# Performance work log

Measured on AMD Instinct MI355X. Metric: run time of the kernel, lower is better.

The kernel has to match this reference:

```python
import jax, jax.numpy as jnp
import numpy as np

CC = 0.25  # commitment cost
K1 = 4096
K2 = 4096
D1 = 64
D2 = 64

def conv1d(x, w, b, stride=1, pad=0):
    # x: [N,C,T], w: [O,I,K] (torch layout)
    y = jax.lax.conv_general_dilated(x, w, (stride,), [(pad, pad)],
                                     dimension_numbers=('NCH', 'OIH', 'NCH'))
    return y + b[None, :, None]

def convT1d(x, w, b, stride=2, pad=1):
    # torch ConvTranspose1d weight layout: [Cin, Cout, K]
    k = w.shape[-1]
    w2 = jnp.flip(w, -1).transpose(1, 0, 2)  # -> [Cout, Cin, K]
    y = jax.lax.conv_general_dilated(x, w2, (1,), [(k - 1 - pad, k - 1 - pad)],
                                     lhs_dilation=(stride,),
                                     dimension_numbers=('NCH', 'OIH', 'NCH'))
    return y + b[None, :, None]

def resblocks(x, w1, b1, w2, b2):
    # w1: [n, C, C, 3], w2: [n, C, C, 1]; n is small & fixed (2)
    for i in range(w1.shape[0]):
        h = conv1d(jax.nn.relu(x), w1[i], b1[i], 1, 1)
        h = conv1d(jax.nn.relu(h), w2[i], b2[i], 1, 0)
        x = x + h
    return x

def quantize(x, embed):
    # x: [B,D,T]; embed: [K,D]
    b, d, t = x.shape
    xf = x.transpose(0, 2, 1).reshape(-1, d)               # [N,D]
    dist = (xf * xf).sum(1, keepdims=True) - 2.0 * (xf @ embed.T) + (embed * embed).sum(1)
    idx = jnp.argmin(dist, axis=1)                          # [N]
    q = embed[idx]                                          # gather == onehot @ embed
    commit = CC * jnp.mean((jax.lax.stop_gradient(q) - xf) ** 2)
    q = xf + jax.lax.stop_gradient(q - xf)                  # straight-through
    q = q.reshape(b, t, d).transpose(0, 2, 1)
    K = embed.shape[0]
    avg = jnp.zeros(K, xf.dtype).at[idx].add(1.0) / xf.shape[0]
    perp = jnp.exp(-jnp.sum(avg * jnp.log(avg + 1e-10)))
    usage = jnp.sum(avg * jnp.log(avg * K + 1e-10))
    return q, commit, perp, usage

def setup_inputs() -> dict:
    key = jax.random.key(0)
    ks = iter(jax.random.split(key, 64))
    def p(*shape):
        return jax.random.normal(next(ks), shape, jnp.float32) * 0.05
    inp = {}
    inp['x'] = jax.random.normal(next(ks), (16, 1, 8192), jnp.float32)
    c1, c2, c3 = 128, 256, 384
    # Encoder
    inp['e_c1_w'] = p(c1, 1, 7);   inp['e_c1_b'] = p(c1)
    inp['e_r1_w1'] = p(2, c1, c1, 3); inp['e_r1_b1'] = p(2, c1)
    inp['e_r1_w2'] = p(2, c1, c1, 1); inp['e_r1_b2'] = p(2, c1)
    inp['e_c2_w'] = p(c2, c1, 5);  inp['e_c2_b'] = p(c2)
    inp['e_r2_w1'] = p(2, c2, c2, 3); inp['e_r2_b1'] = p(2, c2)
    inp['e_r2_w2'] = p(2, c2, c2, 1); inp['e_r2_b2'] = p(2, c2)
    inp['e_c3_w'] = p(c3, c2, 3);  inp['e_c3_b'] = p(c3)
    inp['e_r3_w1'] = p(2, c3, c3, 3); inp['e_r3_b1'] = p(2, c3)
    inp['e_r3_w2'] = p(2, c3, c3, 1); inp['e_r3_b2'] = p(2, c3)
    inp['e_pr_w'] = p(128, c3, 1); inp['e_pr_b'] = p(128)
    # Codebooks (torch.randn init)
    inp['emb1'] = jax.random.normal(next(ks), (K1, D1), jnp.float32)
    inp['emb2'] = jax.random.normal(next(ks), (K2, D2), jnp.float32)
    # Decoder
    inp['d_pr_w'] = p(c3, 128, 1); inp['d_pr_b'] = p(c3)
    inp['d_r1_w1'] = p(2, c3, c3, 3); inp['d_r1_b1'] = p(2, c3)
    inp['d_r1_w2'] = p(2, c3, c3, 1); inp['d_r1_b2'] = p(2, c3)
    inp['d_u1_w'] = p(c3, c2, 4);  inp['d_u1_b'] = p(c2)  # ConvTranspose: [Cin,Cout,K]
    inp['d_r2_w1'] = p(2, c2, c2, 3); inp['d_r2_b1'] = p(2, c2)
    inp['d_r2_w2'] = p(2, c2, c2, 1); inp['d_r2_b2'] = p(2, c2)
    inp['d_u2_w'] = p(c2, c1, 4);  inp['d_u2_b'] = p(c1)
    inp['d_r3_w1'] = p(2, c1, c1, 3); inp['d_r3_b1'] = p(2, c1)
    inp['d_r3_w2'] = p(2, c1, c1, 1); inp['d_r3_b2'] = p(2, c1)
    inp['d_u3_w'] = p(c1, c1, 4);  inp['d_u3_b'] = p(c1)
    inp['d_out_w'] = p(1, c1, 7);  inp['d_out_b'] = p(1)
    return inp

def reference(x, e_c1_w, e_c1_b, e_r1_w1, e_r1_b1, e_r1_w2, e_r1_b2,
              e_c2_w, e_c2_b, e_r2_w1, e_r2_b1, e_r2_w2, e_r2_b2,
              e_c3_w, e_c3_b, e_r3_w1, e_r3_b1, e_r3_w2, e_r3_b2,
              e_pr_w, e_pr_b, emb1, emb2,
              d_pr_w, d_pr_b, d_r1_w1, d_r1_b1, d_r1_w2, d_r1_b2,
              d_u1_w, d_u1_b, d_r2_w1, d_r2_b1, d_r2_w2, d_r2_b2,
              d_u2_w, d_u2_b, d_r3_w1, d_r3_b1, d_r3_w2, d_r3_b2,
              d_u3_w, d_u3_b, d_out_w, d_out_b):
    # Encoder
    z = conv1d(x, e_c1_w, e_c1_b, stride=2, pad=3)
    z = resblocks(z, e_r1_w1, e_r1_b1, e_r1_w2, e_r1_b2)
    z = conv1d(z, e_c2_w, e_c2_b, stride=2, pad=2)
    z = resblocks(z, e_r2_w1, e_r2_b1, e_r2_w2, e_r2_b2)
    z = conv1d(z, e_c3_w, e_c3_b, stride=2, pad=1)
    z = resblocks(z, e_r3_w1, e_r3_b1, e_r3_w2, e_r3_b2)
    z = conv1d(z, e_pr_w, e_pr_b)
    # Product VQ
    q1, c1l, p1, u1 = quantize(z[:, :D1], emb1)
    q2, c2l, p2, u2 = quantize(z[:, D1:], emb2)
    q = jnp.concatenate([q1, q2], axis=1)
    # Decoder
    h = conv1d(q, d_pr_w, d_pr_b)
    h = resblocks(h, d_r1_w1, d_r1_b1, d_r1_w2, d_r1_b2)
    h = convT1d(h, d_u1_w, d_u1_b)
    h = resblocks(h, d_r2_w1, d_r2_b1, d_r2_w2, d_r2_b2)
    h = convT1d(h, d_u2_w, d_u2_b)
    h = resblocks(h, d_r3_w1, d_r3_b1, d_r3_w2, d_r3_b2)
    h = convT1d(h, d_u3_w, d_u3_b)
    x_hat = conv1d(h, d_out_w, d_out_b, stride=1, pad=3)
    return (x_hat, c1l + c2l, u1 + u2, p1, p2)
```

## Files before the change

### kernel.cpp

```cpp
#include <hip/hip_runtime.h>
#include <math.h>

#define TPB 256
typedef __bf16 bf16x8 __attribute__((ext_vector_type(8)));
typedef float f32x4 __attribute__((ext_vector_type(4)));

static __device__ __forceinline__ float bf2f(unsigned short h) {
    union { unsigned int u; float f; } x; x.u = ((unsigned int)h) << 16; return x.f;
}
static __device__ __forceinline__ unsigned short f2bf(float f) {
    union { float f; unsigned int u; } x; x.f = f;
    unsigned int r = x.u + 0x7FFFu + ((x.u >> 16) & 1u);
    return (unsigned short)(r >> 16);
}
static __device__ __forceinline__ unsigned int relu_pk(unsigned int v) {
    unsigned int hi = (v & 0x80000000u) ? 0u : (v & 0xFFFF0000u);
    unsigned int lo = (v & 0x8000u) ? 0u : (v & 0xFFFFu);
    return hi | lo;
}
static __device__ __forceinline__ f32x4 MFMA(bf16x8 a, bf16x8 b, f32x4 c) {
    return __builtin_amdgcn_mfma_f32_16x16x32_bf16(a, b, c, 0, 0, 0);
}

template<int K, bool RELU>
__global__ __launch_bounds__(TPB) void conv1d_k(
    const float* __restrict__ x, const float* __restrict__ w,
    const float* __restrict__ bias, const float* __restrict__ res,
    float* __restrict__ y,
    int N, int Ci, int T, int Co, int To, int stride, int pad)
{
    int id = blockIdx.x * TPB + threadIdx.x;
    int total = N * Co * To;
    if (id >= total) return;
    int to = id % To;
    int co = (id / To) % Co;
    int n  = id / (To * Co);
    const float* xn = x + (size_t)n * Ci * T;
    const float* wc = w + (size_t)co * Ci * K;
    float acc = bias[co];
    int h0 = to * stride - pad;
    for (int ci = 0; ci < Ci; ++ci) {
        const float* xc = xn + (size_t)ci * T;
        const float* wk = wc + (size_t)ci * K;
        #pragma unroll
        for (int k = 0; k < K; ++k) {
            int pos = h0 + k;
            if (pos >= 0 && pos < T) {
                float v = xc[pos];
                if (RELU) v = fmaxf(v, 0.0f);
                acc = fmaf(v, wk[k], acc);
            }
        }
    }
    if (res) acc += res[id];
    y[id] = acc;
}

template<int K, int S, bool RELU, bool RES>
__global__ __launch_bounds__(TPB) void conv_tile_k(
    const float* __restrict__ x, const float* __restrict__ w,
    const float* __restrict__ bias, const float* __restrict__ res,
    float* __restrict__ y, int Ci, int Ti, int Co, int To)
{
    constexpr int CC    = 16;
    constexpr int TNEED = 127 * S + K;
    constexpr int RS    = ((TNEED + 3) & ~3) + 4;
    constexpr int NXV   = 7 * S + K;
    constexpr int NV4   = (NXV + 3) / 4;
    constexpr int WROW  = 68;
    __shared__ float xs[CC][RS];
    __shared__ float ws[CC * K * WROW];

    const int tid   = threadIdx.x;
    const int co_g  = tid & 15;
    const int t_g   = tid >> 4;
    const int tg8S  = t_g * 8 * S;
    const int co_g4 = co_g * 4;
    const int n     = blockIdx.z;
    const int co0   = blockIdx.y * 64;
    const int tb    = blockIdx.x * 128;
    const int t0in  = tb * S - K / 2;

    float4 b4 = *(const float4*)&bias[co0 + co_g4];
    float bi[4] = {b4.x, b4.y, b4.z, b4.w};
    float acc[4][8];
    #pragma unroll
    for (int i = 0; i < 4; ++i)
        #pragma unroll
        for (int j = 0; j < 8; ++j) acc[i][j] = bi[i];

    const int nchunk = Ci / CC;
    for (int ch = 0; ch < nchunk; ++ch) {
        const int ci0 = ch * CC;
        __syncthreads();
        for (int lin = tid; lin < CC * TNEED; lin += TPB) {
            int r = lin / TNEED, off = lin - r * TNEED;
            int t = t0in + off;
            float v = 0.f;
            if (t >= 0 && t < Ti) {
                v = x[((size_t)(n * Ci + ci0 + r)) * Ti + t];
                if (RELU) v = fmaxf(v, 0.f);
            }
            xs[r][off] = v;
        }
        for (int lin = tid; lin < 64 * CC * K; lin += TPB) {
            int co_l = lin / (CC * K), rem = lin - co_l * (CC * K);
            ws[rem * WROW + co_l] =
                w[(size_t)(co0 + co_l) * Ci * K + (size_t)ci0 * K + rem];
        }
        __syncthreads();
        for (int r = 0; r < CC; ++r) {
            float xv[NV4 * 4];
            #pragma unroll
            for (int q = 0; q < NV4; ++q)
                *(float4*)&xv[q * 4] = *(const float4*)&xs[r][tg8S + q * 4];
            #pragma unroll
            for (int k = 0; k < K; ++k) {
                float4 wv = *(const float4*)&ws[(r * K + k) * WROW + co_g4];
                float wa[4] = {wv.x, wv.y, wv.z, wv.w};
                #pragma unroll
                for (int i = 0; i < 4; ++i)
                    #pragma unroll
                    for (int j = 0; j < 8; ++j)
                        acc[i][j] = fmaf(wa[i], xv[j * S + k], acc[i][j]);
            }
        }
    }
    #pragma unroll
    for (int i = 0; i < 4; ++i) {
        size_t yb = ((size_t)(n * Co + co0 + co_g4 + i)) * To + tb + t_g * 8;
        float4 lo = make_float4(acc[i][0], acc[i][1], acc[i][2], acc[i][3]);
        float4 hi = make_float4(acc[i][4], acc[i][5], acc[i][6], acc[i][7]);
        if (RES) {
            float4 r0 = *(const float4*)&res[yb];
            float4 r1 = *(const float4*)&res[yb + 4];
            lo.x += r0.x; lo.y += r0.y; lo.z += r0.z; lo.w += r0.w;
            hi.x += r1.x; hi.y += r1.y; hi.z += r1.z; hi.w += r1.w;
        }
        *(float4*)&y[yb]     = lo;
        *(float4*)&y[yb + 4] = hi;
    }
}

template<int K, int TOFF, bool RELU, bool RES, int OSTR, int OOFF>
__global__ __launch_bounds__(TPB) void gconv_k(
    const unsigned short* __restrict__ x, const unsigned short* __restrict__ wp,
    const float* __restrict__ bias, const unsigned short* __restrict__ res,
    unsigned short* __restrict__ y, int Ci, int Tin, int Co, int Tout)
{
    constexpr int XR = 64 + K - 1;
    __shared__ unsigned short x_lds[XR * 40];
    __shared__ unsigned short w_lds[K * 64 * 40];
    const int tid = threadIdx.x;
    const int n = blockIdx.z, co0 = blockIdx.y * 64, P = blockIdx.x * 64;
    const int wid = tid >> 6, l = tid & 63;
    const int wm = wid >> 1, wn = wid & 1;
    const int lr = l & 15, kg = l >> 4;
    f32x4 acc[2][2] = {{{0.f,0.f,0.f,0.f},{0.f,0.f,0.f,0.f}},
                       {{0.f,0.f,0.f,0.f},{0.f,0.f,0.f,0.f}}};
    const int nch = Ci >> 5;
    for (int cc = 0; cc < nch; ++cc) {
        __syncthreads();
        for (int i = tid; i < XR * 4; i += TPB) {
            int r = i >> 2, c4 = i & 3;
            int gr = P + TOFF + r;
            uint4 v = make_uint4(0u, 0u, 0u, 0u);
            if (gr >= 0 && gr < Tin)
                v = *(const uint4*)(x + ((size_t)(n * Tin + gr) * Ci + cc * 32 + c4 * 8));
            if (RELU) { v.x = relu_pk(v.x); v.y = relu_pk(v.y);
                        v.z = relu_pk(v.z); v.w = relu_pk(v.w); }
            *(uint4*)&x_lds[r * 40 + c4 * 8] = v;
        }
        for (int i = tid; i < K * 64 * 4; i += TPB) {
            int r2 = i >> 2, c4 = i & 3;
            *(uint4*)&w_lds[r2 * 40 + c4 * 8] =
                *(const uint4*)(wp + ((size_t)((r2 >> 6) * Co + co0 + (r2 & 63)) * Ci
                                      + cc * 32 + c4 * 8));
        }
        __syncthreads();
        #pragma unroll
        for (int kk = 0; kk < K; ++kk) {
            bf16x8 av0 = *(const bf16x8*)&x_lds[(wm * 32 +      lr + kk) * 40 + kg * 8];
            bf16x8 av1 = *(const bf16x8*)&x_lds[(wm * 32 + 16 + lr + kk) * 40 + kg * 8];
            bf16x8 bv0 = *(const bf16x8*)&w_lds[(kk * 64 + wn * 32 +      lr) * 40 + kg * 8];
            bf16x8 bv1 = *(const bf16x8*)&w_lds[(kk * 64 + wn * 32 + 16 + lr) * 40 + kg * 8];
            acc[0][0] = MFMA(av0, bv0, acc[0][0]);
            acc[0][1] = MFMA(av0, bv1, acc[0][1]);
            acc[1][0] = MFMA(av1, bv0, acc[1][0]);
            acc[1][1] = MFMA(av1, bv1, acc[1][1]);
        }
    }
    float bb[2] = { bias[co0 + wn * 32 + lr], bias[co0 + wn * 32 + 16 + lr] };
    #pragma unroll
    for (int mf = 0; mf < 2; ++mf)
        #pragma unroll
        for (int nf = 0; nf < 2; ++nf) {
            int co = co0 + wn * 32 + nf * 16 + lr;
            #pragma unroll
            for (int r = 0; r < 4; ++r) {
                int m = wm * 32 + mf * 16 + kg * 4 + r;
                int orow = (P + m) * OSTR + OOFF;
                float v = acc[mf][nf][r] + bb[nf];
                size_t oidx = ((size_t)n * Tout + orow) * Co + co;
                if (RES) v += bf2f(res[oidx]);
                y[oidx] = f2bf(v);
            }
        }
}

__global__ __launch_bounds__(TPB) void gconvt_k(
    const unsigned short* __restrict__ x, const unsigned short* __restrict__ wpe,
    const unsigned short* __restrict__ wpo, const float* __restrict__ bias,
    unsigned short* __restrict__ y, int Ci, int Tin, int Co)
{
    __shared__ unsigned short x_lds[66 * 40];
    __shared__ unsigned short we_lds[2 * 64 * 40];
    __shared__ unsigned short wo_lds[2 * 64 * 40];
    const int tid = threadIdx.x;
    const int n = blockIdx.z, co0 = blockIdx.y * 64, P = blockIdx.x * 64;
    const int wid = tid >> 6, l = tid & 63;
    const int wm = wid >> 1, wn = wid & 1;
    const int lr = l & 15, kg = l >> 4;
    f32x4 accE[2][2] = {{{0.f,0.f,0.f,0.f},{0.f,0.f,0.f,0.f}},
                        {{0.f,0.f,0.f,0.f},{0.f,0.f,0.f,0.f}}};
    f32x4 accO[2][2] = {{{0.f,0.f,0.f,0.f},{0.f,0.f,0.f,0.f}},
                        {{0.f,0.f,0.f,0.f},{0.f,0.f,0.f,0.f}}};
    const int nch = Ci >> 5;
    for (int cc = 0; cc < nch; ++cc) {
        __syncthreads();
        for (int i = tid; i < 66 * 4; i += TPB) {
            int r = i >> 2, c4 = i & 3;
            int gr = P - 1 + r;
            uint4 v = make_uint4(0u, 0u, 0u, 0u);
            if (gr >= 0 && gr < Tin)
                v = *(const uint4*)(x + ((size_t)(n * Tin + gr) * Ci + cc * 32 + c4 * 8));
            *(uint4*)&x_lds[r * 40 + c4 * 8] = v;
        }
        for (int i = tid; i < 2 * 64 * 4; i += TPB) {
            int r2 = i >> 2, c4 = i & 3;
            size_t off = (size_t)((r2 >> 6) * Co + co0 + (r2 & 63)) * Ci + cc * 32 + c4 * 8;
            *(uint4*)&we_lds[r2 * 40 + c4 * 8] = *(const uint4*)(wpe + off);
            *(uint4*)&wo_lds[r2 * 40 + c4 * 8] = *(const uint4*)(wpo + off);
        }
        __syncthreads();
        #pragma unroll
        for (int kk = 0; kk < 2; ++kk) {
            bf16x8 aE0 = *(const bf16x8*)&x_lds[(wm * 32 +      lr + kk) * 40 + kg * 8];
            bf16x8 aE1 = *(const bf16x8*)&x_lds[(wm * 32 + 16 + lr + kk) * 40 + kg * 8];
            bf16x8 bE0 = *(const bf16x8*)&we_lds[(kk * 64 + wn * 32 +      lr) * 40 + kg * 8];
            bf16x8 bE1 = *(const bf16x8*)&we_lds[(kk * 64 + wn * 32 + 16 + lr) * 40 + kg * 8];
            accE[0][0] = MFMA(aE0, bE0, accE[0][0]);
            accE[0][1] = MFMA(aE0, bE1, accE[0][1]);
            accE[1][0] = MFMA(aE1, bE0, accE[1][0]);
            accE[1][1] = MFMA(aE1, bE1, accE[1][1]);
            bf16x8 aO0 = *(const bf16x8*)&x_lds[(wm * 32 +      lr + kk + 1) * 40 + kg * 8];
            bf16x8 aO1 = *(const bf16x8*)&x_lds[(wm * 32 + 16 + lr + kk + 1) * 40 + kg * 8];
            bf16x8 bO0 = *(const bf16x8*)&wo_lds[(kk * 64 + wn * 32 +      lr) * 40 + kg * 8];
            bf16x8 bO1 = *(const bf16x8*)&wo_lds[(kk * 64 + wn * 32 + 16 + lr) * 40 + kg * 8];
            accO[0][0] = MFMA(aO0, bO0, accO[0][0]);
            accO[0][1] = MFMA(aO0, bO1, accO[0][1]);
            accO[1][0] = MFMA(aO1, bO0, accO[1][0]);
            accO[1][1] = MFMA(aO1, bO1, accO[1][1]);
        }
    }
    float bb[2] = { bias[co0 + wn * 32 + lr], bias[co0 + wn * 32 + 16 + lr] };
    #pragma unroll
    for (int mf = 0; mf < 2; ++mf)
        #pragma unroll
        for (int nf = 0; nf < 2; ++nf) {
            int co = co0 + wn * 32 + nf * 16 + lr;
            #pragma unroll
            for (int r = 0; r < 4; ++r) {
                int m = wm * 32 + mf * 16 + kg * 4 + r;
                size_t oe = ((size_t)n * (2 * Tin) + (size_t)(P + m) * 2) * Co + co;
                y[oe]      = f2bf(accE[mf][nf][r] + bb[nf]);
                y[oe + Co] = f2bf(accO[mf][nf][r] + bb[nf]);
            }
        }
}

__global__ __launch_bounds__(TPB) void prep_conv_k(
    const float* __restrict__ w, unsigned short* __restrict__ out, int Co, int Ci, int K)
{
    int id = blockIdx.x * TPB + threadIdx.x;
    if (id >= K * Co * Ci) return;
    int ci = id % Ci, co = (id / Ci) % Co, k = id / (Ci * Co);
    out[id] = f2bf(w[((size_t)co * Ci + ci) * K + k]);
}
__global__ __launch_bounds__(TPB) void prep_convt_k(
    const float* __restrict__ w, unsigned short* __restrict__ oute,
    unsigned short* __restrict__ outo, int Co, int Ci)
{
    int id = blockIdx.x * TPB + threadIdx.x;
    if (id >= 2 * Co * Ci) return;
    int ci = id % Ci, co = (id / Ci) % Co, kp = id / (Ci * Co);
    const float* src = w + ((size_t)ci * Co + co) * 4;
    oute[id] = f2bf(src[3 - 2 * kp]);
    outo[id] = f2bf(src[2 - 2 * kp]);
}

__global__ __launch_bounds__(TPB) void dout_cl_k(
    const unsigned short* __restrict__ x, const float* __restrict__ w,
    const float* __restrict__ b, float* __restrict__ y)
{
    __shared__ unsigned short xs[262 * 40];
    const int tid = threadIdx.x;
    const int tb = blockIdx.x * 256;
    const int n = blockIdx.y;
    float acc = b[0];
    for (int cc = 0; cc < 4; ++cc) {
        __syncthreads();
        for (int i = tid; i < 262 * 4; i += TPB) {
            int r = i >> 2, c4 = i & 3;
            int gr = tb - 3 + r;
            uint4 v = make_uint4(0u, 0u, 0u, 0u);
            if (gr >= 0 && gr < 8192)
                v = *(const uint4*)(x + ((size_t)(n * 8192 + gr) * 128 + cc * 32 + c4 * 8));
            *(uint4*)&xs[r * 40 + c4 * 8] = v;
        }
        __syncthreads();
        #pragma unroll
        for (int k = 0; k < 7; ++k) {
            const unsigned short* row = &xs[(tid + k) * 40];
            #pragma unroll
            for (int e = 0; e < 32; ++e)
                acc = fmaf(bf2f(row[e]), w[(cc * 32 + e) * 7 + k], acc);
        }
    }
    y[(size_t)n * 8192 + tb + tid] = acc;
}

#define NVEC 16384
#define KC   4096
#define DD   64
#define NCH  16

__global__ __launch_bounds__(TPB) void vq_norms_k(
    const float* __restrict__ emb1, const float* __restrict__ emb2,
    float* __restrict__ enorm)
{
    int id = blockIdx.x * TPB + threadIdx.x;
    if (id >= 2 * KC) return;
    const float* e = (id < KC) ? (emb1 + (size_t)id * DD) : (emb2 + (size_t)(id - KC) * DD);
    float s = 0.f;
    #pragma unroll
    for (int d = 0; d < DD; ++d) s = fmaf(e[d], e[d], s);
    enorm[id] = s;
}

__global__ __launch_bounds__(TPB, 3) void vq_partial_k(
    const float* __restrict__ z,
    const float* __restrict__ emb1, const float* __restrict__ emb2,
    const float* __restrict__ enorm,
    float* __restrict__ pmin, int* __restrict__ pidx)
{
    const int v0 = blockIdx.x * (TPB * 2) + threadIdx.x;
    const int v1 = v0 + TPB;
    const int ch = blockIdx.y, cb = blockIdx.z;
    const float* emb = cb ? emb2 : emb1;
    const float* en  = enorm + cb * KC;

    f32x4 xa[16], xb[16];
    {
        int b = v0 >> 10, t = v0 & 1023;
        const float* zp = z + ((size_t)b * 128 + cb * 64) * 1024 + t;
        #pragma unroll
        for (int i = 0; i < 16; ++i) {
            xa[i][0] = zp[(size_t)(4 * i + 0) * 1024];
            xa[i][1] = zp[(size_t)(4 * i + 1) * 1024];
            xa[i][2] = zp[(size_t)(4 * i + 2) * 1024];
            xa[i][3] = zp[(size_t)(4 * i + 3) * 1024];
        }
    }
    {
        int b = v1 >> 10, t = v1 & 1023;
        const float* zp = z + ((size_t)b * 128 + cb * 64) * 1024 + t;
        #pragma unroll
        for (int i = 0; i < 16; ++i) {
            xb[i][0] = zp[(size_t)(4 * i + 0) * 1024];
            xb[i][1] = zp[(size_t)(4 * i + 1) * 1024];
            xb[i][2] = zp[(size_t)(4 * i + 2) * 1024];
            xb[i][3] = zp[(size_t)(4 * i + 3) * 1024];
        }
    }

    float best0 = 1e30f, best1 = 1e30f; int bi0 = 0, bi1 = 0;
    const int c0 = ch * (KC / NCH);
    for (int c = c0; c < c0 + KC / NCH; ++c) {
        const f32x4* e4 = (const f32x4*)(emb + (size_t)c * DD);
        f32x4 pa = {0.f, 0.f, 0.f, 0.f}, pb = {0.f, 0.f, 0.f, 0.f};
        #pragma unroll
        for (int i = 0; i < 16; ++i) {
            f32x4 ev = e4[i];
            pa += xa[i] * ev;
            pb += xb[i] * ev;
        }
        float enc = en[c];
        float sa = enc - 2.0f * ((pa[0] + pa[1]) + (pa[2] + pa[3]));
        float sb = enc - 2.0f * ((pb[0] + pb[1]) + (pb[2] + pb[3]));
        if (sa < best0) { best0 = sa; bi0 = c; }
        if (sb < best1) { best1 = sb; bi1 = c; }
    }
    f32x4 na = {0.f,0.f,0.f,0.f}, nb = {0.f,0.f,0.f,0.f};
    #pragma unroll
    for (int i = 0; i < 16; ++i) { na += xa[i] * xa[i]; nb += xb[i] * xb[i]; }
    float xn0 = (na[0] + na[1]) + (na[2] + na[3]);
    float xn1 = (nb[0] + nb[1]) + (nb[2] + nb[3]);
    size_t base = ((size_t)cb * NCH + ch) * NVEC;
    pmin[base + v0] = best0 + xn0;
    pidx[base + v0] = bi0;
    pmin[base + v1] = best1 + xn1;
    pidx[base + v1] = bi1;
}

__global__ __launch_bounds__(TPB) void vq_finalize_k(
    const float* __restrict__ pmin, const int* __restrict__ pidx,
    int* __restrict__ idxf, float* __restrict__ cnt, float* __restrict__ csum)
{
    int gid = blockIdx.x * TPB + threadIdx.x;
    int cb  = gid >> 14;
    int v   = gid & (NVEC - 1);
    float best = pmin[((size_t)cb * NCH + 0) * NVEC + v];
    int   bi   = pidx[((size_t)cb * NCH + 0) * NVEC + v];
    #pragma unroll
    for (int ch = 1; ch < NCH; ++ch) {
        float m  = pmin[((size_t)cb * NCH + ch) * NVEC + v];
        int   ix = pidx[((size_t)cb * NCH + ch) * NVEC + v];
        if (m < best) { best = m; bi = ix; }
    }
    idxf[cb * NVEC + v] = bi;
    atomicAdd(&cnt[cb * KC + bi], 1.0f);
    float s = best;
    #pragma unroll
    for (int off = 32; off; off >>= 1) s += __shfl_down(s, off, 64);
    __shared__ float wsum[4];
    int wid = threadIdx.x >> 6;
    if ((threadIdx.x & 63) == 0) wsum[wid] = s;
    __syncthreads();
    if (threadIdx.x == 0)
        atomicAdd(&csum[cb], wsum[0] + wsum[1] + wsum[2] + wsum[3]);
}

__global__ __launch_bounds__(TPB) void vq_gather_cl_k(
    const int* __restrict__ idxf,
    const float* __restrict__ emb1, const float* __restrict__ emb2,
    unsigned short* __restrict__ q)
{
    int id = blockIdx.x * TPB + threadIdx.x;
    int c = id & 127;
    int t = (id >> 7) & 1023;
    int n = id >> 17;
    int cb = c >> 6, d = c & 63;
    int idx = idxf[cb * NVEC + n * 1024 + t];
    const float* emb = cb ? emb2 : emb1;
    q[id] = f2bf(emb[(size_t)idx * DD + d]);
}

__global__ __launch_bounds__(TPB) void vq_stats_k(
    const float* __restrict__ cnt, const float* __restrict__ csum,
    float* __restrict__ out)
{
    float h0 = 0.f, h1 = 0.f, u0 = 0.f, u1 = 0.f;
    for (int i = threadIdx.x; i < KC; i += TPB) {
        float a0 = cnt[i]      * (1.0f / NVEC);
        float a1 = cnt[KC + i] * (1.0f / NVEC);
        h0 -= a0 * logf(a0 + 1e-10f);
        h1 -= a1 * logf(a1 + 1e-10f);
        u0 += a0 * logf(a0 * (float)KC + 1e-10f);
        u1 += a1 * logf(a1 * (float)KC + 1e-10f);
    }
    #pragma unroll
    for (int off = 32; off; off >>= 1) {
        h0 += __shfl_down(h0, off, 64);
        h1 += __shfl_down(h1, off, 64);
        u0 += __shfl_down(u0, off, 64);
        u1 += __shfl_down(u1, off, 64);
    }
    __shared__ float red[4][4];
    int wid = threadIdx.x >> 6;
    if ((threadIdx.x & 63) == 0) {
        red[wid][0] = h0; red[wid][1] = h1; red[wid][2] = u0; red[wid][3] = u1;
    }
    __syncthreads();
    if (threadIdx.x == 0) {
        h0 = red[0][0] + red[1][0] + red[2][0] + red[3][0];
        h1 = red[0][1] + red[1][1] + red[2][1] + red[3][1];
        u0 = red[0][2] + red[1][2] + red[2][2] + red[3][2];
        u1 = red[0][3] + red[1][3] + red[2][3] + red[3][3];
        out[0] = 0.25f * (csum[0] + csum[1]) * (1.0f / ((float)NVEC * (float)DD));
        out[1] = u0 + u1;
        out[2] = expf(h0);
        out[3] = expf(h1);
    }
}

template<int K, int S, bool RELU, bool RES>
static void launch_conv(hipStream_t st, const float* x, const float* w, const float* b,
                        const float* res, float* y, int Ci, int Ti, int Co, int To)
{
    dim3 g(To / 128, Co / 64, 16);
    conv_tile_k<K, S, RELU, RES><<<g, TPB, 0, st>>>(x, w, b, res, y, Ci, Ti, Co, To);
}

static void resblocks_t(hipStream_t st, float** cur, float** f1, float** f2,
                        const float* w1, const float* b1, const float* w2, const float* b2,
                        int C, int T)
{
    for (int i = 0; i < 2; ++i) {
        launch_conv<3, 1, true, false>(st, *cur, w1 + (size_t)i * C * C * 3, b1 + i * C,
                                       nullptr, *f1, C, T, C, T);
        launch_conv<1, 1, true, true>(st, *f1, w2 + (size_t)i * C * C, b2 + i * C,
                                      *cur, *f2, C, T, C, T);
        float* t = *cur; *cur = *f2; *f2 = t;
    }
}

template<int K, int TOFF, bool RELU, bool RES, int OSTR, int OOFF>
static void gconv(hipStream_t st, const unsigned short* x, const unsigned short* wp,
                  const float* b, const unsigned short* res, unsigned short* y,
                  int Ci, int Tin, int Co, int Tout)
{
    dim3 g(Tin / 64, Co / 64, 16);
    gconv_k<K, TOFF, RELU, RES, OSTR, OOFF><<<g, TPB, 0, st>>>(x, wp, b, res, y,
                                                               Ci, Tin, Co, Tout);
}

static void gconvt2(hipStream_t st, const unsigned short* x, const unsigned short* we,
                    const unsigned short* wo, const float* b, unsigned short* y,
                    int Ci, int Tin, int Co)
{
    dim3 g(Tin / 64, Co / 64, 16);
    gconvt_k<<<g, TPB, 0, st>>>(x, we, wo, b, y, Ci, Tin, Co);
}

static void dresblock(hipStream_t st, unsigned short* cur, unsigned short* o1,
                      unsigned short* o2, const unsigned short* wpc1,
                      const unsigned short* wpc2, const float* b1, const float* b2,
                      int C, int T)
{
    size_t wc1 = (size_t)3 * C * C, wc2 = (size_t)C * C;
    gconv<3, -1, true, false, 1, 0>(st, cur, wpc1, b1, nullptr, o1, C, T, C, T);
    gconv<1,  0, true, true,  1, 0>(st, o1, wpc2, b2, cur, o2, C, T, C, T);
    gconv<3, -1, true, false, 1, 0>(st, o2, wpc1 + wc1, b1 + C, nullptr, o1, C, T, C, T);
    gconv<1,  0, true, true,  1, 0>(st, o1, wpc2 + wc2, b2 + C, o2, cur, C, T, C, T);
}

static void prep_conv(hipStream_t st, const float* w, unsigned short* out,
                      int Co, int Ci, int K)
{
    int n = K * Co * Ci;
    prep_conv_k<<<(n + TPB - 1) / TPB, TPB, 0, st>>>(w, out, Co, Ci, K);
}
static void prep_convt(hipStream_t st, const float* w, unsigned short* oe,
                       unsigned short* oo, int Co, int Ci)
{
    int n = 2 * Co * Ci;
    prep_convt_k<<<(n + TPB - 1) / TPB, TPB, 0, st>>>(w, oe, oo, Co, Ci);
}

extern "C" void kernel_launch(void* const* d_in, const int* in_sizes, int n_in,
                              void* d_out, int out_size, void* d_ws, size_t ws_size,
                              hipStream_t stream)
{
    const float* x       = (const float*)d_in[0];
    const float* e_c1_w  = (const float*)d_in[1];
    const float* e_c1_b  = (const float*)d_in[2];
    const float* e_r1_w1 = (const float*)d_in[3];
    const float* e_r1_b1 = (const float*)d_in[4];
    const float* e_r1_w2 = (const float*)d_in[5];
    const float* e_r1_b2 = (const float*)d_in[6];
    const float* e_c2_w  = (const float*)d_in[7];
    const float* e_c2_b  = (const float*)d_in[8];
    const float* e_r2_w1 = (const float*)d_in[9];
    const float* e_r2_b1 = (const float*)d_in[10];
    const float* e_r2_w2 = (const float*)d_in[11];
    const float* e_r2_b2 = (const float*)d_in[12];
    const float* e_c3_w  = (const float*)d_in[13];
    const float* e_c3_b  = (const float*)d_in[14];
    const float* e_r3_w1 = (const float*)d_in[15];
    const float* e_r3_b1 = (const float*)d_in[16];
    const float* e_r3_w2 = (const float*)d_in[17];
    const float* e_r3_b2 = (const float*)d_in[18];
    const float* e_pr_w  = (const float*)d_in[19];
    const float* e_pr_b  = (const float*)d_in[20];
    const float* emb1    = (const float*)d_in[21];
    const float* emb2    = (const float*)d_in[22];
    const float* d_pr_w  = (const float*)d_in[23];
    const float* d_pr_b  = (const float*)d_in[24];
    const float* d_r1_w1 = (const float*)d_in[25];
    const float* d_r1_b1 = (const float*)d_in[26];
    const float* d_r1_w2 = (const float*)d_in[27];
    const float* d_r1_b2 = (const float*)d_in[28];
    const float* d_u1_w  = (const float*)d_in[29];
    const float* d_u1_b  = (const float*)d_in[30];
    const float* d_r2_w1 = (const float*)d_in[31];
    const float* d_r2_b1 = (const float*)d_in[32];
    const float* d_r2_w2 = (const float*)d_in[33];
    const float* d_r2_b2 = (const float*)d_in[34];
    const float* d_u2_w  = (const float*)d_in[35];
    const float* d_u2_b  = (const float*)d_in[36];
    const float* d_r3_w1 = (const float*)d_in[37];
    const float* d_r3_b1 = (const float*)d_in[38];
    const float* d_r3_w2 = (const float*)d_in[39];
    const float* d_r3_b2 = (const float*)d_in[40];
    const float* d_u3_w  = (const float*)d_in[41];
    const float* d_u3_b  = (const float*)d_in[42];
    const float* d_outw  = (const float*)d_in[43];
    const float* d_outb  = (const float*)d_in[44];

    const size_t BUF = 16777216;
    float* W0   = (float*)d_ws;
    float* W1   = W0 + BUF;
    float* W2   = W1 + BUF;
    float* pmin = W2 + BUF;
    int*   pidx = (int*)(pmin + 524288);
    int*   idxf = pidx + 524288;
    float* enorm= (float*)(idxf + 32768);
    float* cnt  = enorm + 8192;
    float* csum = cnt + 8192;
    unsigned short* wp = (unsigned short*)(csum + 4);

    unsigned short* wp_dpr  = wp;
    unsigned short* wp_r1c1 = wp_dpr  + 49152;
    unsigned short* wp_r1c2 = wp_r1c1 + 884736;
    unsigned short* wp_u1e  = wp_r1c2 + 294912;
    unsigned short* wp_u1o  = wp_u1e  + 196608;
    unsigned short* wp_r2c1 = wp_u1o  + 196608;
    unsigned short* wp_r2c2 = wp_r2c1 + 393216;
    unsigned short* wp_u2e  = wp_r2c2 + 131072;
    unsigned short* wp_u2o  = wp_u2e  + 65536;
    unsigned short* wp_r3c1 = wp_u2o  + 65536;
    unsigned short* wp_r3c2 = wp_r3c1 + 98304;
    unsigned short* wp_u3e  = wp_r3c2 + 32768;
    unsigned short* wp_u3o  = wp_u3e  + 32768;

    unsigned short* bfA = (unsigned short*)W0;
    unsigned short* bfB = bfA + BUF;
    unsigned short* bfC = (unsigned short*)W2;

    float *A = W0, *B = W1, *C = W2, *t_;
    hipStream_t st = stream;

    prep_conv(st, d_pr_w, wp_dpr, 384, 128, 1);
    prep_conv(st, d_r1_w1,                      wp_r1c1,          384, 384, 3);
    prep_conv(st, d_r1_w1 + (size_t)384*384*3,  wp_r1c1 + 442368, 384, 384, 3);
    prep_conv(st, d_r1_w2,                      wp_r1c2,          384, 384, 1);
    prep_conv(st, d_r1_w2 + (size_t)384*384,    wp_r1c2 + 147456, 384, 384, 1);
    prep_convt(st, d_u1_w, wp_u1e, wp_u1o, 256, 384);
    prep_conv(st, d_r2_w1,                      wp_r2c1,          256, 256, 3);
    prep_conv(st, d_r2_w1 + (size_t)256*256*3,  wp_r2c1 + 196608, 256, 256, 3);
    prep_conv(st, d_r2_w2,                      wp_r2c2,          256, 256, 1);
    prep_conv(st, d_r2_w2 + (size_t)256*256,    wp_r2c2 + 65536,  256, 256, 1);
    prep_convt(st, d_u2_w, wp_u2e, wp_u2o, 128, 256);
    prep_conv(st, d_r3_w1,                      wp_r3c1,          128, 128, 3);
    prep_conv(st, d_r3_w1 + (size_t)128*128*3,  wp_r3c1 + 49152,  128, 128, 3);
    prep_conv(st, d_r3_w2,                      wp_r3c2,          128, 128, 1);
    prep_conv(st, d_r3_w2 + (size_t)128*128,    wp_r3c2 + 16384,  128, 128, 1);
    prep_convt(st, d_u3_w, wp_u3e, wp_u3o, 128, 128);

    {
        int total = 16 * 128 * 4096;
        conv1d_k<7, false><<<(total + TPB - 1) / TPB, TPB, 0, st>>>(
            x, e_c1_w, e_c1_b, nullptr, A, 16, 1, 8192, 128, 4096, 2, 3);
    }
    resblocks_t(st, &A, &B, &C, e_r1_w1, e_r1_b1, e_r1_w2, e_r1_b2, 128, 4096);
    launch_conv<5, 2, false, false>(st, A, e_c2_w, e_c2_b, nullptr, B, 128, 4096, 256, 2048);
    t_ = A; A = B; B = t_;
    resblocks_t(st, &A, &B, &C, e_r2_w1, e_r2_b1, e_r2_w2, e_r2_b2, 256, 2048);
    launch_conv<3, 2, false, false>(st, A, e_c3_w, e_c3_b, nullptr, B, 256, 2048, 384, 1024);
    t_ = A; A = B; B = t_;
    resblocks_t(st, &A, &B, &C, e_r3_w1, e_r3_b1, e_r3_w2, e_r3_b2, 384, 1024);
    launch_conv<1, 1, false, false>(st, A, e_pr_w, e_pr_b, nullptr, B, 384, 1024, 128, 1024);
    t_ = A; A = B; B = t_;

    hipMemsetAsync(cnt, 0, (8192 + 4) * sizeof(float), st);
    vq_norms_k<<<(2 * KC + TPB - 1) / TPB, TPB, 0, st>>>(emb1, emb2, enorm);
    dim3 pg(NVEC / (TPB * 2), NCH, 2);
    vq_partial_k<<<pg, TPB, 0, st>>>(A, emb1, emb2, enorm, pmin, pidx);
    vq_finalize_k<<<2 * NVEC / TPB, TPB, 0, st>>>(pmin, pidx, idxf, cnt, csum);
    vq_gather_cl_k<<<16 * 1024 * 128 / TPB, TPB, 0, st>>>(idxf, emb1, emb2, bfA);

    gconv<1, 0, false, false, 1, 0>(st, bfA, wp_dpr, d_pr_b, nullptr, bfB,
                                    128, 1024, 384, 1024);
    dresblock(st, bfB, bfA, bfC, wp_r1c1, wp_r1c2, d_r1_b1, d_r1_b2, 384, 1024);
    gconvt2(st, bfB, wp_u1e, wp_u1o, d_u1_b, bfA, 384, 1024, 256);
    dresblock(st, bfA, bfB, bfC, wp_r2c1, wp_r2c2, d_r2_b1, d_r2_b2, 256, 2048);
    gconvt2(st, bfA, wp_u2e, wp_u2o, d_u2_b, bfB, 256, 2048, 128);
    dresblock(st, bfB, bfA, bfC, wp_r3c1, wp_r3c2, d_r3_b1, d_r3_b2, 128, 4096);
    gconvt2(st, bfB, wp_u3e, wp_u3o, d_u3_b, bfA, 128, 4096, 128);
    {
        dim3 g(8192 / 256, 16);
        dout_cl_k<<<g, TPB, 0, st>>>(bfA, d_outw, d_outb, (float*)d_out);
    }

    vq_stats_k<<<1, TPB, 0, st>>>(cnt, csum, (float*)d_out + 131072);
}
```

Baseline: 3.082 ms.

## Widen fp32 encoder conv tiles to 16 outputs per thread with input-channel split

The fp32 encoder conv kernel now computes 16 time steps per thread (256-wide block tile) instead of 8, doubling register reuse of each loaded weight. To keep enough blocks in flight with the larger tile, most convolutions split the input-channel reduction into two sequential launches, where the second reads back and accumulates into the partial output. This raises register pressure, which may lower occupancy, and adds an extra launch plus a read-modify-write of the output per split conv.

New measurement: 3.978 ms. 29.1% more time.

```diff
diff --git a/kernel.cpp b/kernel.cpp
--- a/kernel.cpp
+++ b/kernel.cpp
@@ -56,16 +56,19 @@
     y[id] = acc;
 }
 
-template<int K, int S, bool RELU, bool RES>
-__global__ __launch_bounds__(TPB) void conv_tile_k(
+template<int K, int S, bool RELU, bool RES, bool FIRST>
+__global__ __launch_bounds__(TPB) void conv_tile16_k(
     const float* __restrict__ x, const float* __restrict__ w,
     const float* __restrict__ bias, const float* __restrict__ res,
-    float* __restrict__ y, int Ci, int Ti, int Co, int To)
-{
+    float* __restrict__ y, int Ci, int Ti, int Co, int To,
+    int cibeg, int ciend)
+{
+    constexpr int TT    = 256;
+    constexpr int TPT   = 16;
     constexpr int CC    = 16;
-    constexpr int TNEED = 127 * S + K;
+    constexpr int TNEED = (TT - 1) * S + K;
     constexpr int RS    = ((TNEED + 3) & ~3) + 4;
-    constexpr int NXV   = 7 * S + K;
+    constexpr int NXV   = (TPT - 1) * S + K;
     constexpr int NV4   = (NXV + 3) / 4;
     constexpr int WROW  = 68;
     __shared__ float xs[CC][RS];
@@ -74,24 +77,29 @@
     const int tid   = threadIdx.x;
     const int co_g  = tid & 15;
     const int t_g   = tid >> 4;
-    const int tg8S  = t_g * 8 * S;
+    const int tcol0 = t_g * TPT * S;
     const int co_g4 = co_g * 4;
     const int n     = blockIdx.z;
     const int co0   = blockIdx.y * 64;
-    const int tb    = blockIdx.x * 128;
+    const int tb    = blockIdx.x * TT;
     const int t0in  = tb * S - K / 2;
 
-    float4 b4 = *(const float4*)&bias[co0 + co_g4];
-    float bi[4] = {b4.x, b4.y, b4.z, b4.w};
-    float acc[4][8];
-    #pragma unroll
-    for (int i = 0; i < 4; ++i)
-        #pragma unroll
-        for (int j = 0; j < 8; ++j) acc[i][j] = bi[i];
-
-    const int nchunk = Ci / CC;
-    for (int ch = 0; ch < nchunk; ++ch) {
-        const int ci0 = ch * CC;
+    float acc[4][TPT];
+    if (FIRST) {
+        float4 b4 = *(const float4*)&bias[co0 + co_g4];
+        float bi[4] = {b4.x, b4.y, b4.z, b4.w};
+        #pragma unroll
+        for (int i = 0; i < 4; ++i)
+            #pragma unroll
+            for (int j = 0; j < TPT; ++j) acc[i][j] = bi[i];
+    } else {
+        #pragma unroll
+        for (int i = 0; i < 4; ++i)
+            #pragma unroll
+            for (int j = 0; j < TPT; ++j) acc[i][j] = 0.f;
+    }
+
+    for (int ci0 = cibeg; ci0 < ciend; ci0 += CC) {
         __syncthreads();
         for (int lin = tid; lin < CC * TNEED; lin += TPB) {
             int r = lin / TNEED, off = lin - r * TNEED;
@@ -113,7 +121,7 @@
             float xv[NV4 * 4];
             #pragma unroll
             for (int q = 0; q < NV4; ++q)
-                *(float4*)&xv[q * 4] = *(const float4*)&xs[r][tg8S + q * 4];
+                *(float4*)&xv[q * 4] = *(const float4*)&xs[r][tcol0 + q * 4];
             #pragma unroll
             for (int k = 0; k < K; ++k) {
                 float4 wv = *(const float4*)&ws[(r * K + k) * WROW + co_g4];
@@ -121,24 +129,27 @@
                 #pragma unroll
                 for (int i = 0; i < 4; ++i)
                     #pragma unroll
-                    for (int j = 0; j < 8; ++j)
+                    for (int j = 0; j < TPT; ++j)
                         acc[i][j] = fmaf(wa[i], xv[j * S + k], acc[i][j]);
             }
         }
     }
     #pragma unroll
     for (int i = 0; i < 4; ++i) {
-        size_t yb = ((size_t)(n * Co + co0 + co_g4 + i)) * To + tb + t_g * 8;
-        float4 lo = make_float4(acc[i][0], acc[i][1], acc[i][2], acc[i][3]);
-        float4 hi = make_float4(acc[i][4], acc[i][5], acc[i][6], acc[i][7]);
-        if (RES) {
-            float4 r0 = *(const float4*)&res[yb];
-            float4 r1 = *(const float4*)&res[yb + 4];
-            lo.x += r0.x; lo.y += r0.y; lo.z += r0.z; lo.w += r0.w;
-            hi.x += r1.x; hi.y += r1.y; hi.z += r1.z; hi.w += r1.w;
-        }
-        *(float4*)&y[yb]     = lo;
-        *(float4*)&y[yb + 4] = hi;
+        size_t yb = ((size_t)(n * Co + co0 + co_g4 + i)) * To + tb + t_g * TPT;
+        #pragma unroll
+        for (int q = 0; q < 4; ++q) {
+            float4 v = make_float4(acc[i][q*4], acc[i][q*4+1], acc[i][q*4+2], acc[i][q*4+3]);
+            if (!FIRST) {
+                float4 o = *(const float4*)&y[yb + q * 4];
+                v.x += o.x; v.y += o.y; v.z += o.z; v.w += o.w;
+            }
+            if (RES) {
+                float4 r0 = *(const float4*)&res[yb + q * 4];
+                v.x += r0.x; v.y += r0.y; v.z += r0.z; v.w += r0.w;
+            }
+            *(float4*)&y[yb + q * 4] = v;
+        }
     }
 }
 
@@ -495,22 +506,32 @@
 }
 
 template<int K, int S, bool RELU, bool RES>
-static void launch_conv(hipStream_t st, const float* x, const float* w, const float* b,
-                        const float* res, float* y, int Ci, int Ti, int Co, int To)
-{
-    dim3 g(To / 128, Co / 64, 16);
-    conv_tile_k<K, S, RELU, RES><<<g, TPB, 0, st>>>(x, w, b, res, y, Ci, Ti, Co, To);
-}
-
-static void resblocks_t(hipStream_t st, float** cur, float** f1, float** f2,
+static void launch_conv16(hipStream_t st, const float* x, const float* w, const float* b,
+                          const float* res, float* y, int Ci, int Ti, int Co, int To,
+                          int split)
+{
+    dim3 g(To / 256, Co / 64, 16);
+    if (split == 1) {
+        conv_tile16_k<K, S, RELU, RES, true><<<g, TPB, 0, st>>>(
+            x, w, b, res, y, Ci, Ti, Co, To, 0, Ci);
+    } else {
+        int h = Ci / 2;
+        conv_tile16_k<K, S, RELU, false, true><<<g, TPB, 0, st>>>(
+            x, w, b, nullptr, y, Ci, Ti, Co, To, 0, h);
+        conv_tile16_k<K, S, RELU, RES, false><<<g, TPB, 0, st>>>(
+            x, w, b, res, y, Ci, Ti, Co, To, h, Ci);
+    }
+}
+
+static void resblocks16(hipStream_t st, float** cur, float** f1, float** f2,
                         const float* w1, const float* b1, const float* w2, const float* b2,
-                        int C, int T)
+                        int C, int T, int split)
 {
     for (int i = 0; i < 2; ++i) {
-        launch_conv<3, 1, true, false>(st, *cur, w1 + (size_t)i * C * C * 3, b1 + i * C,
-                                       nullptr, *f1, C, T, C, T);
-        launch_conv<1, 1, true, true>(st, *f1, w2 + (size_t)i * C * C, b2 + i * C,
-                                      *cur, *f2, C, T, C, T);
+        launch_conv16<3, 1, true, false>(st, *cur, w1 + (size_t)i * C * C * 3, b1 + i * C,
+                                         nullptr, *f1, C, T, C, T, split);
+        launch_conv16<1, 1, true, true>(st, *f1, w2 + (size_t)i * C * C, b2 + i * C,
+                                        *cur, *f2, C, T, C, T, split);
         float* t = *cur; *cur = *f2; *f2 = t;
     }
 }
@@ -663,14 +684,17 @@
         conv1d_k<7, false><<<(total + TPB - 1) / TPB, TPB, 0, st>>>(
             x, e_c1_w, e_c1_b, nullptr, A, 16, 1, 8192, 128, 4096, 2, 3);
     }
-    resblocks_t(st, &A, &B, &C, e_r1_w1, e_r1_b1, e_r1_w2, e_r1_b2, 128, 4096);
-    launch_conv<5, 2, false, false>(st, A, e_c2_w, e_c2_b, nullptr, B, 128, 4096, 256, 2048);
+    resblocks16(st, &A, &B, &C, e_r1_w1, e_r1_b1, e_r1_w2, e_r1_b2, 128, 4096, 2);
+    launch_conv16<5, 2, false, false>(st, A, e_c2_w, e_c2_b, nullptr, B,
+                                      128, 4096, 256, 2048, 1);
     t_ = A; A = B; B = t_;
-    resblocks_t(st, &A, &B, &C, e_r2_w1, e_r2_b1, e_r2_w2, e_r2_b2, 256, 2048);
-    launch_conv<3, 2, false, false>(st, A, e_c3_w, e_c3_b, nullptr, B, 256, 2048, 384, 1024);
+    resblocks16(st, &A, &B, &C, e_r2_w1, e_r2_b1, e_r2_w2, e_r2_b2, 256, 2048, 2);
+    launch_conv16<3, 2, false, false>(st, A, e_c3_w, e_c3_b, nullptr, B,
+                                      256, 2048, 384, 1024, 2);
     t_ = A; A = B; B = t_;
-    resblocks_t(st, &A, &B, &C, e_r3_w1, e_r3_b1, e_r3_w2, e_r3_b2, 384, 1024);
-    launch_conv<1, 1, false, false>(st, A, e_pr_w, e_pr_b, nullptr, B, 384, 1024, 128, 1024);
+    resblocks16(st, &A, &B, &C, e_r3_w1, e_r3_b1, e_r3_w2, e_r3_b2, 384, 1024, 2);
+    launch_conv16<1, 1, false, false>(st, A, e_pr_w, e_pr_b, nullptr, B,
+                                      384, 1024, 128, 1024, 2);
     t_ = A; A = B; B = t_;
 
     hipMemsetAsync(cnt, 0, (8192 + 4) * sizeof(float), st);
```
